# Performance work log

Hardware: AMD Instinct MI355X
Metric: run time of the kernel (lower is better)

Reference implementation:

```python
import jax, jax.numpy as jnp
import numpy as np

N_NODES = 50000
N_EDGES = 800000
D_IN = 128
D_HID = 128


def _sage_conv(x, src, dst, W_l, b_l, W_r, num_nodes):
    # PyG SAGEConv (mean aggr): out = lin_l(mean_{j in N(i)} x_j) + lin_r(x_i)
    msgs = x[src]  # [E, d] irregular gather
    agg = jax.ops.segment_sum(msgs, dst, num_segments=num_nodes)  # [N, d]
    cnt = jax.ops.segment_sum(jnp.ones((dst.shape[0], 1), x.dtype), dst, num_segments=num_nodes)
    agg = agg / jnp.maximum(cnt, 1.0)  # mean over in-neighbors
    return agg @ W_l.T + b_l + x @ W_r.T


def setup_inputs() -> dict:
    key = jax.random.key(0)
    ks = jax.random.split(key, 8)
    x = jax.random.normal(ks[0], (N_NODES, D_IN), dtype=jnp.float32)
    edge_index = jax.random.randint(ks[1], (2, N_EDGES), 0, N_NODES, dtype=jnp.int64)
    s0 = 1.0 / np.sqrt(D_IN)
    s1 = 1.0 / np.sqrt(D_HID)
    return {
        "x": x,
        "edge_index": edge_index,
        "W_l0": jax.random.uniform(ks[2], (D_HID, D_IN), jnp.float32, -s0, s0),
        "b_l0": jnp.zeros((D_HID,), jnp.float32),
        "W_r0": jax.random.uniform(ks[3], (D_HID, D_IN), jnp.float32, -s0, s0),
        "W_l1": jax.random.uniform(ks[4], (D_HID, D_HID), jnp.float32, -s1, s1),
        "b_l1": jnp.zeros((D_HID,), jnp.float32),
        "W_r1": jax.random.uniform(ks[5], (D_HID, D_HID), jnp.float32, -s1, s1),
    }


def reference(x, edge_index, W_l0, b_l0, W_r0, W_l1, b_l1, W_r1):
    src, dst = edge_index[0], edge_index[1]
    n = x.shape[0]
    # layer 0 + ReLU (dropout is identity at inference)
    h = _sage_conv(x, src, dst, W_l0, b_l0, W_r0, n)
    h = jax.nn.relu(h)
    # layer 1 (no activation on last layer)
    out = _sage_conv(h, src, dst, W_l1, b_l1, W_r1, n)
    return out
```

## Files before the change

### kernel.cpp

```cpp
#include <hip/hip_runtime.h>


typedef __attribute__((ext_vector_type(8))) short short8;
typedef __attribute__((ext_vector_type(4))) float f32x4;
typedef __attribute__((ext_vector_type(2))) float f32x2;

#define DEV __device__ __forceinline__

DEV unsigned short f2b(float f) {
  unsigned u = __builtin_bit_cast(unsigned, f);
  u += 0x7fffu + ((u >> 16) & 1u);
  return (unsigned short)(u >> 16);
}
DEV float b2f(unsigned short h) {
  unsigned u = ((unsigned)h) << 16;
  return __builtin_bit_cast(float, u);
}
DEV float bitf(unsigned u) { return __builtin_bit_cast(float, u); }

constexpr int N_NODES = 50000;
constexpr int N_EDGES = 800000;
constexpr int D = 128;
constexpr int NBUCK = (N_NODES + 255) / 256;
constexpr int BCAP = 5120;
constexpr int NBIN = 784;
constexpr int EPB = (N_EDGES + NBIN - 1) / NBIN;
constexpr int NCONV = (N_NODES * D / 4) / 256;
constexpr int NPREP = (2 * 32 * 128) / 256;

__global__ __launch_bounds__(256) void setup_kernel(
    const float* __restrict__ x, unsigned short* __restrict__ xb,
    const float* __restrict__ Wl0, const float* __restrict__ Wr0,
    const float* __restrict__ Wl1, const float* __restrict__ Wr1,
    unsigned short* __restrict__ Bf,
    const int* __restrict__ src, const int* __restrict__ dst,
    int* __restrict__ g_bcnt, unsigned* __restrict__ staging) {
  __shared__ int cnt[NBUCK];
  __shared__ int cur[NBUCK];
  int bid = blockIdx.x;
  int t = threadIdx.x;

  if (bid < NBIN) {
    for (int i = t; i < NBUCK; i += 256) cnt[i] = 0;
    __syncthreads();
    int beg = bid * EPB;
    int end = min(beg + EPB, N_EDGES);
    for (int e = beg + t; e < end; e += 256) {
      atomicAdd(&cnt[dst[e] >> 8], 1);
    }
    __syncthreads();
    for (int i = t; i < NBUCK; i += 256) {
      cur[i] = atomicAdd(&g_bcnt[i], cnt[i]);
    }
    __syncthreads();
    for (int e = beg + t; e < end; e += 256) {
      int d = dst[e];
      int b = d >> 8;
      int p = atomicAdd(&cur[b], 1);
      if (p >= BCAP) p = BCAP - 1;
      staging[b * BCAP + p] = ((unsigned)(d & 255) << 16) | (unsigned)src[e];
    }
    return;
  }
  if (bid < NBIN + NCONV) {
    int i = (bid - NBIN) * 256 + t;
    f32x4 v = ((const f32x4*)x)[i];
    uint2 o;
    o.x = (unsigned)f2b(v.x) | ((unsigned)f2b(v.y) << 16);
    o.y = (unsigned)f2b(v.z) | ((unsigned)f2b(v.w) << 16);
    ((uint2*)xb)[i] = o;
    return;
  }
  int f = (bid - NBIN - NCONV) * 256 + t;
  int layer = f >> 12;
  int kchunk = (f >> 7) & 31;
  int n = f & 127;
  const float* W;
  if (layer == 0) W = (kchunk < 16) ? Wl0 : Wr0;
  else            W = (kchunk < 16) ? Wl1 : Wr1;
  int k = (kchunk & 15) * 8;
  const f32x4* row = (const f32x4*)(W + n * D + k);
  f32x4 a = row[0], b = row[1];
  uint4 pk;
  pk.x = (unsigned)f2b(a.x) | ((unsigned)f2b(a.y) << 16);
  pk.y = (unsigned)f2b(a.z) | ((unsigned)f2b(a.w) << 16);
  pk.z = (unsigned)f2b(b.x) | ((unsigned)f2b(b.y) << 16);
  pk.w = (unsigned)f2b(b.z) | ((unsigned)f2b(b.w) << 16);
  *(uint4*)(Bf + (size_t)f * 8) = pk;
}

__global__ __launch_bounds__(1024) void fill2_kernel(const unsigned* __restrict__ staging,
                                                     const int* __restrict__ g_bcnt,
                                                     int* __restrict__ offs,
                                                     int* __restrict__ csr) {
  __shared__ int cnts[256];
  __shared__ int tmp[256];
  __shared__ int hist[256];
  __shared__ int cur[256];
  __shared__ int sh_n, sh_bb;
  int b = blockIdx.x;
  int t = threadIdx.x;
  if (t < 256) {
    int c = (t < NBUCK) ? g_bcnt[t] : 0;
    cnts[t] = c;
    tmp[t] = c;
    hist[t] = 0;
  }
  __syncthreads();
  if (t < 256) {
    for (int off = 1; off < 256; off <<= 1) {
      int u = (t >= off) ? tmp[t - off] : 0;
      __syncthreads();
      tmp[t] += u;
      __syncthreads();
    }
  } else {
    for (int off = 1; off < 256; off <<= 1) { __syncthreads(); __syncthreads(); }
  }
  if (t == 0) {
    sh_n = cnts[b];
    sh_bb = tmp[b] - cnts[b];
  }
  __syncthreads();
  int n = sh_n;
  int bb = sh_bb;
  if (b == 0 && t == 0) offs[N_NODES] = N_EDGES;

  const unsigned* st = staging + b * BCAP;
  for (int e = t; e < n; e += 1024) atomicAdd(&hist[st[e] >> 16], 1);
  __syncthreads();
  if (t < 256) {
    int v = hist[t];
    tmp[t] = v;
    __syncthreads();
    for (int off = 1; off < 256; off <<= 1) {
      int u = (t >= off) ? tmp[t - off] : 0;
      __syncthreads();
      tmp[t] += u;
      __syncthreads();
    }
    int excl = tmp[t] - v;
    int node = b * 256 + t;
    if (node < N_NODES) offs[node] = bb + excl;
    cur[t] = bb + excl;
  } else {
    __syncthreads();
    for (int off = 1; off < 256; off <<= 1) { __syncthreads(); __syncthreads(); }
  }
  __syncthreads();
  for (int e = t; e < n; e += 1024) {
    unsigned pk = st[e];
    int p = atomicAdd(&cur[pk >> 16], 1);
    csr[p] = (int)(pk & 0xffffu);
  }
}

__global__ __launch_bounds__(256) void agg_kernel(
    const unsigned short* __restrict__ feat,
    const int* __restrict__ csr_src,
    const int* __restrict__ offs,
    unsigned short* __restrict__ out) {
  int wv = __builtin_amdgcn_readfirstlane((int)(threadIdx.x >> 6));
  int w = (int)blockIdx.x * 4 + wv;
  int lane = threadIdx.x & 63;
  if (w >= N_NODES) return;
  int s = __builtin_amdgcn_readfirstlane(offs[w]);
  int e = __builtin_amdgcn_readfirstlane(offs[w + 1]);
  int deg = e - s;
  const unsigned* f = (const unsigned*)feat;
  const int* p = csr_src + s;
  f32x2 acc = {0.f, 0.f};

  if (deg <= 31) {
    unsigned u[32];
#pragma unroll
    for (int jb = 0; jb < 32; jb += 4) {
      if (jb < deg) {
#pragma unroll
        for (int j2 = 0; j2 < 4; ++j2) {
          unsigned sj = (unsigned)p[jb + j2] & 0xFFFFu;
          u[jb + j2] = f[(sj << 6) + lane];
        }
      }
    }
#pragma unroll
    for (int j = 0; j < 32; ++j) {
      if (j < deg) {
        f32x2 v = {bitf(u[j] << 16), bitf(u[j] & 0xffff0000u)};
        acc += v;
      }
    }
  } else {
    int c = 0;
    for (; c + 16 <= deg; c += 16) {
      unsigned u[16];
#pragma unroll
      for (int j = 0; j < 16; ++j) {
        int sj = p[c + j];
        u[j] = f[((unsigned)sj << 6) + lane];
      }
#pragma unroll
      for (int j = 0; j < 16; ++j) {
        f32x2 v = {bitf(u[j] << 16), bitf(u[j] & 0xffff0000u)};
        acc += v;
      }
    }
    int nb = deg - c;
    unsigned u[16];
#pragma unroll
    for (int j = 0; j < 16; ++j) {
      if (j < nb) {
        int sj = p[c + j];
        u[j] = f[((unsigned)sj << 6) + lane];
      }
    }
#pragma unroll
    for (int j = 0; j < 16; ++j) {
      if (j < nb) {
        f32x2 v = {bitf(u[j] << 16), bitf(u[j] & 0xffff0000u)};
        acc += v;
      }
    }
  }

  float inv = 1.0f / (float)max(deg, 1);
  unsigned o = (unsigned)f2b(acc.x * inv) | ((unsigned)f2b(acc.y * inv) << 16);
  ((unsigned*)out)[(size_t)w * 64 + lane] = o;
}

__global__ __launch_bounds__(256) void gemm_kernel(
    const unsigned short* __restrict__ Aagg,
    const unsigned short* __restrict__ Afeat,
    const unsigned short* __restrict__ Bf,
    const float* __restrict__ bias,
    float* __restrict__ out_f32,
    unsigned short* __restrict__ out_bf16,
    int relu_bf16) {
  int wave = threadIdx.x >> 6;
  int lane = threadIdx.x & 63;
  int ml = lane & 15;
  int quad = lane >> 4;
  int node0 = blockIdx.x * 64 + wave * 16;

  int arow = node0 + ml;
  if (arow >= N_NODES) arow = N_NODES - 1;

  f32x4 acc[8];
#pragma unroll
  for (int t = 0; t < 8; ++t) acc[t] = (f32x4){0.f, 0.f, 0.f, 0.f};

  const short8* bf8 = (const short8*)Bf;
#pragma unroll
  for (int mat = 0; mat < 2; ++mat) {
    const unsigned short* A = mat ? Afeat : Aagg;
    const short8* arow8 = (const short8*)(A + (size_t)arow * D);
    int kbase = mat * 16;
#pragma unroll
    for (int kc = 0; kc < 4; ++kc) {
      short8 af = arow8[kc * 4 + quad];
      int kchunk = kbase + kc * 4 + quad;
      const short8* brow = bf8 + kchunk * 128;
#pragma unroll
      for (int nt = 0; nt < 8; ++nt) {
        short8 bfr = brow[nt * 16 + ml];
        acc[nt] = __builtin_amdgcn_mfma_f32_16x16x32_bf16(af, bfr, acc[nt], 0, 0, 0);
      }
    }
  }

#pragma unroll
  for (int nt = 0; nt < 8; ++nt) {
    int col = nt * 16 + ml;
    float bv = bias[col];
#pragma unroll
    for (int r = 0; r < 4; ++r) {
      int node = node0 + quad * 4 + r;
      if (node >= N_NODES) continue;
      float v = acc[nt][r] + bv;
      if (relu_bf16) {
        v = v > 0.f ? v : 0.f;
        out_bf16[(size_t)node * D + col] = f2b(v);
      } else {
        out_f32[(size_t)node * D + col] = v;
      }
    }
  }
}

extern "C" void kernel_launch(void* const* d_in, const int* in_sizes, int n_in,
                              void* d_out, int out_size, void* d_ws, size_t ws_size,
                              hipStream_t stream) {
  const float* x   = (const float*)d_in[0];
  const int*   ei  = (const int*)d_in[1];
  const float* Wl0 = (const float*)d_in[2];
  const float* bl0 = (const float*)d_in[3];
  const float* Wr0 = (const float*)d_in[4];
  const float* Wl1 = (const float*)d_in[5];
  const float* bl1 = (const float*)d_in[6];
  const float* Wr1 = (const float*)d_in[7];
  float* out = (float*)d_out;

  char* ws = (char*)d_ws;
  size_t o = 0;
  auto carve = [&](size_t bytes) {
    char* p = ws + o;
    o += bytes;
    o = (o + 255) & ~(size_t)255;
    return p;
  };
  int* offs       = (int*)carve((size_t)(N_NODES + 1) * 4);
  int* csr        = (int*)carve((size_t)N_EDGES * 4);
  int* g_bcnt     = (int*)carve((size_t)NBUCK * 4);
  unsigned* staging = (unsigned*)carve((size_t)NBUCK * BCAP * 4);
  unsigned short* Bf   = (unsigned short*)carve((size_t)2 * 32 * 128 * 8 * 2);
  unsigned short* xb   = (unsigned short*)carve((size_t)N_NODES * D * 2);
  unsigned short* aggb = (unsigned short*)carve((size_t)N_NODES * D * 2);
  unsigned short* hb   = (unsigned short*)carve((size_t)N_NODES * D * 2);

  const int* srcp = ei;
  const int* dstp = ei + N_EDGES;

  hipMemsetAsync(g_bcnt, 0, (size_t)NBUCK * 4, stream);
  setup_kernel<<<NBIN + NCONV + NPREP, 256, 0, stream>>>(
      x, xb, Wl0, Wr0, Wl1, Wr1, Bf, srcp, dstp, g_bcnt, staging);
  fill2_kernel<<<NBUCK, 1024, 0, stream>>>(staging, g_bcnt, offs, csr);

  const int GEMM_BLOCKS = (N_NODES + 63) / 64;
  agg_kernel<<<(N_NODES + 3) / 4, 256, 0, stream>>>(xb, csr, offs, aggb);
  gemm_kernel<<<GEMM_BLOCKS, 256, 0, stream>>>(aggb, xb, Bf, bl0, nullptr, hb, 1);
  agg_kernel<<<(N_NODES + 3) / 4, 256, 0, stream>>>(hb, csr, offs, aggb);
  gemm_kernel<<<GEMM_BLOCKS, 256, 0, stream>>>(aggb, hb, Bf + 32 * 128 * 8, bl1,
                                               out, nullptr, 0);
}
```

Before: 206.4 us.

## Replace global bucket atomics with per-bin staging slots and counts matrix

Edge binning now writes each block's edges into a private fixed-capacity slot per destination bucket and records per-bin counts, in place of reserving space through global atomics on a shared bucket counter. This removes the memset and the global atomic contention. The fill kernel sums the counts column to get bucket totals and reads each bin's slot in one thread per bin. The cost is a serial loop of 784 count reads per bucket thread, uncoalesced per-thread staging reads, and a fixed capacity of 40 edges per bin and bucket. Any overflow beyond that is silently dropped, which only holds for the expected random-degree distribution.

```diff
diff --git a/kernel.cpp b/kernel.cpp
--- a/kernel.cpp
+++ b/kernel.cpp
@@ -22,9 +22,9 @@
 constexpr int N_EDGES = 800000;
 constexpr int D = 128;
 constexpr int NBUCK = (N_NODES + 255) / 256;
-constexpr int BCAP = 5120;
 constexpr int NBIN = 784;
 constexpr int EPB = (N_EDGES + NBIN - 1) / NBIN;
+constexpr int SCAP = 40;
 constexpr int NCONV = (N_NODES * D / 4) / 256;
 constexpr int NPREP = (2 * 32 * 128) / 256;
 
@@ -34,14 +34,14 @@
     const float* __restrict__ Wl1, const float* __restrict__ Wr1,
     unsigned short* __restrict__ Bf,
     const int* __restrict__ src, const int* __restrict__ dst,
-    int* __restrict__ g_bcnt, unsigned* __restrict__ staging) {
+    int* __restrict__ counts, unsigned* __restrict__ staging) {
   __shared__ int cnt[NBUCK];
   __shared__ int cur[NBUCK];
   int bid = blockIdx.x;
   int t = threadIdx.x;
 
   if (bid < NBIN) {
-    for (int i = t; i < NBUCK; i += 256) cnt[i] = 0;
+    for (int i = t; i < NBUCK; i += 256) { cnt[i] = 0; cur[i] = 0; }
     __syncthreads();
     int beg = bid * EPB;
     int end = min(beg + EPB, N_EDGES);
@@ -50,15 +50,15 @@
     }
     __syncthreads();
     for (int i = t; i < NBUCK; i += 256) {
-      cur[i] = atomicAdd(&g_bcnt[i], cnt[i]);
-    }
-    __syncthreads();
+      counts[bid * NBUCK + i] = min(cnt[i], SCAP);
+    }
     for (int e = beg + t; e < end; e += 256) {
       int d = dst[e];
       int b = d >> 8;
       int p = atomicAdd(&cur[b], 1);
-      if (p >= BCAP) p = BCAP - 1;
-      staging[b * BCAP + p] = ((unsigned)(d & 255) << 16) | (unsigned)src[e];
+      if (p < SCAP)
+        staging[((size_t)bid * NBUCK + b) * SCAP + p] =
+            ((unsigned)(d & 255) << 16) | (unsigned)src[e];
     }
     return;
   }
@@ -90,21 +90,33 @@
 }
 
 __global__ __launch_bounds__(1024) void fill2_kernel(const unsigned* __restrict__ staging,
-                                                     const int* __restrict__ g_bcnt,
+                                                     const int* __restrict__ counts,
                                                      int* __restrict__ offs,
                                                      int* __restrict__ csr) {
-  __shared__ int cnts[256];
+  __shared__ int totals[256];
   __shared__ int tmp[256];
   __shared__ int hist[256];
   __shared__ int cur[256];
   __shared__ int sh_n, sh_bb;
   int b = blockIdx.x;
   int t = threadIdx.x;
+  if (t < 256) hist[t] = 0;
+  __syncthreads();
+
+  int myc = 0;
+  const unsigned* sl = nullptr;
+  if (t < NBIN) {
+    myc = counts[t * NBUCK + b];
+    sl = staging + ((size_t)t * NBUCK + b) * SCAP;
+    for (int k = 0; k < myc; ++k) atomicAdd(&hist[sl[k] >> 16], 1);
+  }
   if (t < 256) {
-    int c = (t < NBUCK) ? g_bcnt[t] : 0;
-    cnts[t] = c;
-    tmp[t] = c;
-    hist[t] = 0;
+    int s = 0;
+    if (t < NBUCK) {
+      for (int r = 0; r < NBIN; ++r) s += counts[r * NBUCK + t];
+    }
+    totals[t] = s;
+    tmp[t] = s;
   }
   __syncthreads();
   if (t < 256) {
@@ -118,17 +130,14 @@
     for (int off = 1; off < 256; off <<= 1) { __syncthreads(); __syncthreads(); }
   }
   if (t == 0) {
-    sh_n = cnts[b];
-    sh_bb = tmp[b] - cnts[b];
+    sh_n = totals[b];
+    sh_bb = tmp[b] - totals[b];
   }
   __syncthreads();
-  int n = sh_n;
   int bb = sh_bb;
+  (void)sh_n;
   if (b == 0 && t == 0) offs[N_NODES] = N_EDGES;
 
-  const unsigned* st = staging + b * BCAP;
-  for (int e = t; e < n; e += 1024) atomicAdd(&hist[st[e] >> 16], 1);
-  __syncthreads();
   if (t < 256) {
     int v = hist[t];
     tmp[t] = v;
@@ -148,10 +157,12 @@
     for (int off = 1; off < 256; off <<= 1) { __syncthreads(); __syncthreads(); }
   }
   __syncthreads();
-  for (int e = t; e < n; e += 1024) {
-    unsigned pk = st[e];
-    int p = atomicAdd(&cur[pk >> 16], 1);
-    csr[p] = (int)(pk & 0xffffu);
+  if (t < NBIN) {
+    for (int k = 0; k < myc; ++k) {
+      unsigned pk = sl[k];
+      int p = atomicAdd(&cur[pk >> 16], 1);
+      csr[p] = (int)(pk & 0xffffu);
+    }
   }
 }
 
@@ -310,8 +321,8 @@
   };
   int* offs       = (int*)carve((size_t)(N_NODES + 1) * 4);
   int* csr        = (int*)carve((size_t)N_EDGES * 4);
-  int* g_bcnt     = (int*)carve((size_t)NBUCK * 4);
-  unsigned* staging = (unsigned*)carve((size_t)NBUCK * BCAP * 4);
+  int* counts     = (int*)carve((size_t)NBIN * NBUCK * 4);
+  unsigned* staging = (unsigned*)carve((size_t)NBIN * NBUCK * SCAP * 4);
   unsigned short* Bf   = (unsigned short*)carve((size_t)2 * 32 * 128 * 8 * 2);
   unsigned short* xb   = (unsigned short*)carve((size_t)N_NODES * D * 2);
   unsigned short* aggb = (unsigned short*)carve((size_t)N_NODES * D * 2);
@@ -320,10 +331,9 @@
   const int* srcp = ei;
   const int* dstp = ei + N_EDGES;
 
-  hipMemsetAsync(g_bcnt, 0, (size_t)NBUCK * 4, stream);
   setup_kernel<<<NBIN + NCONV + NPREP, 256, 0, stream>>>(
-      x, xb, Wl0, Wr0, Wl1, Wr1, Bf, srcp, dstp, g_bcnt, staging);
-  fill2_kernel<<<NBUCK, 1024, 0, stream>>>(staging, g_bcnt, offs, csr);
+      x, xb, Wl0, Wr0, Wl1, Wr1, Bf, srcp, dstp, counts, staging);
+  fill2_kernel<<<NBUCK, 1024, 0, stream>>>(staging, counts, offs, csr);
 
   const int GEMM_BLOCKS = (N_NODES + 63) / 64;
   agg_kernel<<<(N_NODES + 3) / 4, 256, 0, stream>>>(xb, csr, offs, aggb);
```

Result: slower. 220.5 us (+6.8%).
